# Kernel optimization log

Hardware: AMD Instinct MI355X
Metric: run time of the kernel (lower is better)

The kernel has to match this reference:

```python
import jax, jax.numpy as jnp
import numpy as np

D_FEAT = 6
HIDDEN = 64
NEG_SLOPE = 0.01  # torch LeakyReLU default


def gru_layer(x, Wih, Whh, bih, bhh):
    # x: [N, T, D] -> outputs [N, T, H], PyTorch GRU gate math (r,z,n order)
    N = x.shape[0]
    H = Whh.shape[1]
    def step(h, xt):
        gi = xt @ Wih.T + bih          # [N, 3H]
        gh = h @ Whh.T + bhh           # [N, 3H]
        i_r, i_z, i_n = jnp.split(gi, 3, axis=-1)
        h_r, h_z, h_n = jnp.split(gh, 3, axis=-1)
        r = jax.nn.sigmoid(i_r + h_r)
        z = jax.nn.sigmoid(i_z + h_z)
        n = jnp.tanh(i_n + r * h_n)
        h_new = (1.0 - z) * n + z * h
        return h_new, h_new
    h0 = jnp.zeros((N, H), x.dtype)
    _, hs = jax.lax.scan(step, h0, jnp.swapaxes(x, 0, 1))  # hs: [T, N, H]
    return jnp.swapaxes(hs, 0, 1)


def setup_inputs() -> dict:
    key = jax.random.key(0)
    ks = jax.random.split(key, 16)
    N, T, D, H, R = 2048, 60, D_FEAT, HIDDEN, 20
    x = jax.random.normal(ks[0], (N, D * T), dtype=jnp.float32)
    vals = jax.random.uniform(ks[1], (N, N, R), dtype=jnp.float32)
    keep = jax.random.uniform(ks[2], (N, N, R), dtype=jnp.float32) < 0.3
    relation_matrix = vals * keep.astype(jnp.float32)
    s = 1.0 / np.sqrt(H)
    def u(k, shape):
        return jax.random.uniform(k, shape, dtype=jnp.float32, minval=-s, maxval=s)
    inp = {
        "x": x,
        "relation_matrix": relation_matrix,
        "Wih0": u(ks[3], (3 * H, D)),
        "Whh0": u(ks[4], (3 * H, H)),
        "bih0": u(ks[5], (3 * H,)),
        "bhh0": u(ks[6], (3 * H,)),
        "Wih1": u(ks[7], (3 * H, H)),
        "Whh1": u(ks[8], (3 * H, H)),
        "bih1": u(ks[9], (3 * H,)),
        "bhh1": u(ks[10], (3 * H,)),
        "W": jax.random.normal(ks[11], (2 * H + R, 1), dtype=jnp.float32) * 0.1,
        "b": jnp.zeros((1,), dtype=jnp.float32),
        "fc_w": u(ks[12], (1, H)),
        "fc_b": jnp.zeros((1,), dtype=jnp.float32),
    }
    return inp


def reference(x, relation_matrix, Wih0, Whh0, bih0, bhh0, Wih1, Whh1, bih1, bhh1, W, b, fc_w, fc_b):
    N = x.shape[0]
    H = HIDDEN
    R = relation_matrix.shape[2]
    # [N, d_feat*T] -> [N, T, d_feat]
    xs = jnp.transpose(x.reshape(N, D_FEAT, -1), (0, 2, 1))
    h = gru_layer(xs, Wih0, Whh0, bih0, bhh0)
    h = gru_layer(h, Wih1, Whh1, bih1, bhh1)
    x_hidden = h[:, -1, :]  # [N, H]
    # decompose concat @ W:  W = [W1 (ei part); W2 (hidden part); W3 (relation part)]
    W1 = W[:H, 0]
    W2 = W[H:2 * H, 0]
    W3 = W[2 * H:, 0]
    ai = x_hidden @ W1          # [N] contribution of row i
    aj = x_hidden @ W2          # [N] contribution of col j
    ar = jnp.einsum('ijr,r->ij', relation_matrix, W3)  # [N, N]
    weight = ai[:, None] + aj[None, :] + ar + b[0]
    weight = jnp.where(weight >= 0, weight, NEG_SLOPE * weight)  # leaky_relu
    mask = (jnp.sum(relation_matrix, axis=2) != 0).astype(x_hidden.dtype)
    valid_weight = mask * weight
    valid_weight = jax.nn.softmax(valid_weight, axis=1)
    hidden = valid_weight @ x_hidden  # [N, H]
    pred_all = ((hidden + x_hidden) @ fc_w.T + fc_b).squeeze(-1)  # [N]
    return pred_all
```

## Files before the change

kernel.cpp:

```cpp
#include <hip/hip_runtime.h>
#include <cstddef>

typedef __attribute__((ext_vector_type(8))) short short8;
typedef __attribute__((ext_vector_type(4))) float f32x4;

#define MFMA16(a, b, c) __builtin_amdgcn_mfma_f32_16x16x32_bf16((a), (b), (c), 0, 0, 0)

__device__ __forceinline__ unsigned short f2bf(float f) {
    unsigned u = __float_as_uint(f);
    u = (u + 0x7fffu + ((u >> 16) & 1u)) >> 16;
    return (unsigned short)u;
}
__device__ __forceinline__ float bf2f(unsigned short s) {
    return __uint_as_float(((unsigned)s) << 16);
}
__device__ __forceinline__ float sigm(float v) { return 1.f / (1.f + __expf(-v)); }
__device__ __forceinline__ float tanh_(float v) {
    float a = fabsf(v);
    float e = __expf(-2.f * a);
    float t = (1.f - e) / (1.f + e);
    return v < 0.f ? -t : t;
}

typedef __attribute__((address_space(1))) const void gas_t;
typedef __attribute__((address_space(3))) void las_t;
__device__ __forceinline__ void gld_lds16(const void* g, void* l) {
    __builtin_amdgcn_global_load_lds((gas_t*)g, (las_t*)l, 16, 0, 0);
}

__launch_bounds__(768, 3)
__global__ void gru_kernel(const float* __restrict__ x,
                           const float* __restrict__ Wih0, const float* __restrict__ Whh0,
                           const float* __restrict__ bih0, const float* __restrict__ bhh0,
                           const float* __restrict__ Wih1, const float* __restrict__ Whh1,
                           const float* __restrict__ bih1, const float* __restrict__ bhh1,
                           float* __restrict__ xhid) {
    __shared__ __align__(16) unsigned short h0h[2][1024], h0l[2][1024];
    __shared__ __align__(16) unsigned short h1h[2][1024], h1l[2][1024];
    __shared__ __align__(16) float P1[2][16][195];
    __shared__ __align__(16) short8 axbuf[2400];

    const int tid  = threadIdx.x;
    const int grp  = tid >> 8;
    const int lane = tid & 63;
    const int gw   = (tid >> 6) & 3;
    const int c    = lane & 15;
    const int q    = lane >> 4;
    const int jj   = gw * 16 + c;

    for (int i = tid; i < 1024; i += 768) {
        h0h[0][i] = 0; h0l[0][i] = 0; h1h[0][i] = 0; h1l[0][i] = 0;
    }
    {
        const float* xb = x + (size_t)blockIdx.x * 8 * 360;
        for (int f = tid; f < 1920; f += 768) {
            const int t = f >> 5, s = (f >> 2) & 7, qq = f & 3;
            unsigned short Hh[6], Ll[6];
#pragma unroll
            for (int d = 0; d < 6; ++d) {
                const float v = xb[s * 360 + d * 60 + t];
                Hh[d] = f2bf(v); Ll[d] = f2bf(v - bf2f(Hh[d]));
            }
            short8 fr;
#pragma unroll
            for (int e = 0; e < 8; ++e) {
                const int k = qq * 8 + e;
                unsigned short u = 0;
                if (k < 6) u = Hh[k];
                else if (k < 12) u = Ll[k - 6];
                else if (k < 18) u = Hh[k - 12];
                fr[e] = (short)u;
            }
            axbuf[t * 40 + s * 5 + qq] = fr;
        }
    }

    const int ka    = q * 8;
    const int swzA0 = c * 64 + (ka ^ ((c & 7) << 3));
    const int swzA1 = c * 64 + ((32 + ka) ^ ((c & 7) << 3));

    __syncthreads();

    if (grp == 0) {
        short8 Bhh[3][2], Bhl[3][2], Bc[3];
#pragma unroll
        for (int g = 0; g < 3; ++g) {
            const int o = g * 64 + jj;
#pragma unroll
            for (int kt = 0; kt < 2; ++kt) {
                const int k0 = kt * 32 + q * 8;
#pragma unroll
                for (int e = 0; e < 8; ++e) {
                    const float v = Whh0[o * 64 + k0 + e];
                    const unsigned short hi = f2bf(v);
                    Bhh[g][kt][e] = (short)hi; Bhl[g][kt][e] = (short)f2bf(v - bf2f(hi));
                }
            }
#pragma unroll
            for (int e = 0; e < 8; ++e) {
                const int ks = q * 8 + e;
                unsigned short bv = 0;
                if (ks < 6)       bv = f2bf(Wih0[o * 6 + ks]);
                else if (ks < 12) bv = f2bf(Wih0[o * 6 + ks - 6]);
                else if (ks < 18) {
                    const float v = Wih0[o * 6 + ks - 12];
                    const unsigned short hi = f2bf(v);
                    bv = f2bf(v - bf2f(hi));
                }
                Bc[g][e] = (short)bv;
            }
        }
        const float br = bih0[jj] + bhh0[jj];
        const float bz = bih0[64 + jj] + bhh0[64 + jj];
        const float bi = bih0[128 + jj];
        const float bh = bhh0[128 + jj];
        float hreg[4] = {0.f, 0.f, 0.f, 0.f};

        for (int it = 0; it < 62; ++it) {
            if (it < 60) {
                const int par = it & 1;
                const short8 ah0 = *(const short8*)&h0h[par][swzA0];
                const short8 ah1 = *(const short8*)&h0h[par][swzA1];
                const short8 al0 = *(const short8*)&h0l[par][swzA0];
                const short8 al1 = *(const short8*)&h0l[par][swzA1];
                const short8 ax  = axbuf[it * 40 + (c & 7) * 5 + q];

                f32x4 accr = {br, br, br, br};
                f32x4 accz = {bz, bz, bz, bz};
                f32x4 acci = {bi, bi, bi, bi};
                f32x4 acch = {bh, bh, bh, bh};

                accr = MFMA16(ah0, Bhh[0][0], accr); accr = MFMA16(ah1, Bhh[0][1], accr);
                accr = MFMA16(al0, Bhh[0][0], accr); accr = MFMA16(al1, Bhh[0][1], accr);
                accr = MFMA16(ah0, Bhl[0][0], accr); accr = MFMA16(ah1, Bhl[0][1], accr);
                accr = MFMA16(ax, Bc[0], accr);

                accz = MFMA16(ah0, Bhh[1][0], accz); accz = MFMA16(ah1, Bhh[1][1], accz);
                accz = MFMA16(al0, Bhh[1][0], accz); accz = MFMA16(al1, Bhh[1][1], accz);
                accz = MFMA16(ah0, Bhl[1][0], accz); accz = MFMA16(ah1, Bhl[1][1], accz);
                accz = MFMA16(ax, Bc[1], accz);

                acci = MFMA16(ax, Bc[2], acci);

                acch = MFMA16(ah0, Bhh[2][0], acch); acch = MFMA16(ah1, Bhh[2][1], acch);
                acch = MFMA16(al0, Bhh[2][0], acch); acch = MFMA16(al1, Bhh[2][1], acch);
                acch = MFMA16(ah0, Bhl[2][0], acch); acch = MFMA16(ah1, Bhl[2][1], acch);

#pragma unroll
                for (int i2 = 0; i2 < 4; ++i2) {
                    const float rr = sigm(accr[i2]);
                    const float zz = sigm(accz[i2]);
                    const float nn = tanh_(acci[i2] + rr * acch[i2]);
                    const float hv = (1.f - zz) * nn + zz * hreg[i2];
                    hreg[i2] = hv;
                    const int r  = q * 4 + i2;
                    const int ix = r * 64 + (jj ^ ((r & 7) << 3));
                    const unsigned short hi = f2bf(hv);
                    h0h[par ^ 1][ix] = hi;
                    h0l[par ^ 1][ix] = f2bf(hv - bf2f(hi));
                }
            }
            __syncthreads();
        }
    } else if (grp == 1) {
        short8 Bih[3][2], Bil[3][2];
#pragma unroll
        for (int g = 0; g < 3; ++g) {
            const int o = g * 64 + jj;
#pragma unroll
            for (int kt = 0; kt < 2; ++kt) {
                const int k0 = kt * 32 + q * 8;
#pragma unroll
                for (int e = 0; e < 8; ++e) {
                    const float v = Wih1[o * 64 + k0 + e];
                    const unsigned short hi = f2bf(v);
                    Bih[g][kt][e] = (short)hi; Bil[g][kt][e] = (short)f2bf(v - bf2f(hi));
                }
            }
        }
        const float br = bih1[jj] + bhh1[jj];
        const float bz = bih1[64 + jj] + bhh1[64 + jj];
        const float bi = bih1[128 + jj];

        for (int it = 0; it < 62; ++it) {
            if (it >= 1 && it < 61) {
                const int par = it & 1;
                const short8 gh0 = *(const short8*)&h0h[par][swzA0];
                const short8 gh1 = *(const short8*)&h0h[par][swzA1];
                const short8 gl0 = *(const short8*)&h0l[par][swzA0];
                const short8 gl1 = *(const short8*)&h0l[par][swzA1];

                f32x4 ar = {br, br, br, br};
                f32x4 az = {bz, bz, bz, bz};
                f32x4 an = {bi, bi, bi, bi};

                ar = MFMA16(gh0, Bih[0][0], ar); ar = MFMA16(gh1, Bih[0][1], ar);
                ar = MFMA16(gl0, Bih[0][0], ar); ar = MFMA16(gl1, Bih[0][1], ar);
                ar = MFMA16(gh0, Bil[0][0], ar); ar = MFMA16(gh1, Bil[0][1], ar);

                az = MFMA16(gh0, Bih[1][0], az); az = MFMA16(gh1, Bih[1][1], az);
                az = MFMA16(gl0, Bih[1][0], az); az = MFMA16(gl1, Bih[1][1], az);
                az = MFMA16(gh0, Bil[1][0], az); az = MFMA16(gh1, Bil[1][1], az);

                an = MFMA16(gh0, Bih[2][0], an); an = MFMA16(gh1, Bih[2][1], an);
                an = MFMA16(gl0, Bih[2][0], an); an = MFMA16(gl1, Bih[2][1], an);
                an = MFMA16(gh0, Bil[2][0], an); an = MFMA16(gh1, Bil[2][1], an);

#pragma unroll
                for (int i2 = 0; i2 < 4; ++i2) {
                    const int r = q * 4 + i2;
                    P1[par][r][jj]       = ar[i2];
                    P1[par][r][64 + jj]  = az[i2];
                    P1[par][r][128 + jj] = an[i2];
                }
            }
            __syncthreads();
        }
    } else {
        short8 Bhh[3][2], Bhl[3][2];
#pragma unroll
        for (int g = 0; g < 3; ++g) {
            const int o = g * 64 + jj;
#pragma unroll
            for (int kt = 0; kt < 2; ++kt) {
                const int k0 = kt * 32 + q * 8;
#pragma unroll
                for (int e = 0; e < 8; ++e) {
                    const float v = Whh1[o * 64 + k0 + e];
                    const unsigned short hi = f2bf(v);
                    Bhh[g][kt][e] = (short)hi; Bhl[g][kt][e] = (short)f2bf(v - bf2f(hi));
                }
            }
        }
        const float bh = bhh1[128 + jj];
        float hreg[4] = {0.f, 0.f, 0.f, 0.f};

        for (int it = 0; it < 62; ++it) {
            if (it >= 2) {
                const int par = it & 1;
                const short8 hh0 = *(const short8*)&h1h[par][swzA0];
                const short8 hh1_ = *(const short8*)&h1h[par][swzA1];
                const short8 hl0 = *(const short8*)&h1l[par][swzA0];
                const short8 hl1_ = *(const short8*)&h1l[par][swzA1];

                float p1r[4], p1z[4], p1n[4];
#pragma unroll
                for (int i2 = 0; i2 < 4; ++i2) {
                    const int r = q * 4 + i2;
                    p1r[i2] = P1[par ^ 1][r][jj];
                    p1z[i2] = P1[par ^ 1][r][64 + jj];
                    p1n[i2] = P1[par ^ 1][r][128 + jj];
                }

                f32x4 ar  = {p1r[0], p1r[1], p1r[2], p1r[3]};
                f32x4 az  = {p1z[0], p1z[1], p1z[2], p1z[3]};
                f32x4 ahn = {bh, bh, bh, bh};

                ar = MFMA16(hh0, Bhh[0][0], ar); ar = MFMA16(hh1_, Bhh[0][1], ar);
                ar = MFMA16(hl0, Bhh[0][0], ar); ar = MFMA16(hl1_, Bhh[0][1], ar);
                ar = MFMA16(hh0, Bhl[0][0], ar); ar = MFMA16(hh1_, Bhl[0][1], ar);

                az = MFMA16(hh0, Bhh[1][0], az); az = MFMA16(hh1_, Bhh[1][1], az);
                az = MFMA16(hl0, Bhh[1][0], az); az = MFMA16(hl1_, Bhh[1][1], az);
                az = MFMA16(hh0, Bhl[1][0], az); az = MFMA16(hh1_, Bhl[1][1], az);

                ahn = MFMA16(hh0, Bhh[2][0], ahn); ahn = MFMA16(hh1_, Bhh[2][1], ahn);
                ahn = MFMA16(hl0, Bhh[2][0], ahn); ahn = MFMA16(hl1_, Bhh[2][1], ahn);
                ahn = MFMA16(hh0, Bhl[2][0], ahn); ahn = MFMA16(hh1_, Bhl[2][1], ahn);

#pragma unroll
                for (int i2 = 0; i2 < 4; ++i2) {
                    const float rr = sigm(ar[i2]);
                    const float zz = sigm(az[i2]);
                    const float nn = tanh_(p1n[i2] + rr * ahn[i2]);
                    const float hv = (1.f - zz) * nn + zz * hreg[i2];
                    hreg[i2] = hv;
                    const int r  = q * 4 + i2;
                    const int ix = r * 64 + (jj ^ ((r & 7) << 3));
                    const unsigned short hi = f2bf(hv);
                    h1h[par ^ 1][ix] = hi;
                    h1l[par ^ 1][ix] = f2bf(hv - bf2f(hi));
                    if (it == 61 && q < 2)
                        xhid[((size_t)blockIdx.x * 8 + r) * 64 + jj] = hv;
                }
            }
            __syncthreads();
        }
    }
}

__global__ void aij_kernel(const float* __restrict__ xh, const float* __restrict__ W,
                           float* __restrict__ ai, float* __restrict__ aj) {
    const int n = blockIdx.x * 256 + threadIdx.x;
    const float* row = xh + (size_t)n * 64;
    float a1 = 0.f, a2 = 0.f;
#pragma unroll
    for (int k = 0; k < 64; k += 4) {
        const f32x4 v = *(const f32x4*)(row + k);
#pragma unroll
        for (int u = 0; u < 4; ++u) {
            a1 += v[u] * W[k + u];
            a2 += v[u] * W[64 + k + u];
        }
    }
    ai[n] = a1;
    aj[n] = a2;
}

__launch_bounds__(256, 2)
__global__ void rel_kernel(const float* __restrict__ rel, const float* __restrict__ xh,
                           const float* __restrict__ ai, const float* __restrict__ aj,
                           const float* __restrict__ W, const float* __restrict__ bptr,
                           const float* __restrict__ fcw, const float* __restrict__ fcb,
                           float* __restrict__ out) {
    __shared__ __align__(16) unsigned char stage[2][2][10240];
    __shared__ __align__(16) float pexp[2][2048];
    __shared__ __align__(16) float aj_s[2048];
    __shared__ float w3b_s[24];
    __shared__ float hidpart[4][2][64];
    __shared__ float redm[2][2], reds[2][2], rinv_s[2];

    const int tid  = threadIdx.x;
    const int lane = tid & 63;
    const int wv   = tid >> 6;
    const int i0   = blockIdx.x * 2;

    for (int k = tid; k < 2048; k += 256) aj_s[k] = aj[k];
    if (tid < 20) w3b_s[tid] = W[128 + tid];
    if (tid == 20) w3b_s[20] = bptr[0];
    if (tid < 2)  w3b_s[21 + tid] = ai[i0 + tid];
    __syncthreads();

    float w3[20];
#pragma unroll
    for (int r = 0; r < 20; ++r) w3[r] = w3b_s[r];
    const float bb  = w3b_s[20];
    const float aiv = (tid >> 7) ? w3b_s[22] : w3b_s[21];

    const int r_ = tid >> 7;
    const int t7 = tid & 127;

#pragma unroll
    for (int k = 0; k < 5; ++k) {
        const int m = wv + 4 * k;
        const int rr = m / 10, oo = (m % 10) * 1024;
        const unsigned char* g =
            (const unsigned char*)(rel + (size_t)(i0 + rr) * 2048 * 20) + oo + lane * 16;
        gld_lds16(g, &stage[0][rr][oo]);
    }

    for (int c = 0; c < 16; ++c) {
        const int buf = c & 1;
        if (c < 15) {
#pragma unroll
            for (int k = 0; k < 5; ++k) {
                const int m = wv + 4 * k;
                const int rr = m / 10, oo = (m % 10) * 1024;
                const unsigned char* g =
                    (const unsigned char*)(rel + ((size_t)(i0 + rr) * 2048 + (size_t)(c + 1) * 128) * 20)
                    + oo + lane * 16;
                gld_lds16(g, &stage[buf ^ 1][rr][oo]);
            }
            asm volatile("s_waitcnt vmcnt(5)" ::: "memory");
        } else {
            asm volatile("s_waitcnt vmcnt(0)" ::: "memory");
        }
        __builtin_amdgcn_s_barrier();
        __builtin_amdgcn_sched_barrier(0);

        const unsigned char* sp = &stage[buf][r_][t7 * 80];
        float arv = 0.f, ms = 0.f;
#pragma unroll
        for (int e = 0; e < 5; ++e) {
            const f32x4 v = *(const f32x4*)(sp + e * 16);
            arv += v[0] * w3[e * 4] + v[1] * w3[e * 4 + 1]
                 + v[2] * w3[e * 4 + 2] + v[3] * w3[e * 4 + 3];
            ms += v[0] + v[1] + v[2] + v[3];
        }
        const int j = c * 128 + t7;
        float wvv = aiv + aj_s[j] + arv + bb;
        wvv = (wvv >= 0.f) ? wvv : 0.01f * wvv;
        pexp[r_][j] = (ms != 0.f) ? wvv : 0.f;
        __builtin_amdgcn_s_barrier();
    }
    __syncthreads();

    const int c7 = tid & 127;
    const int wh = (tid >> 6) & 1;
    float mx = -1e30f;
#pragma unroll
    for (int m = 0; m < 16; ++m) mx = fmaxf(mx, pexp[r_][c7 + 128 * m]);
#pragma unroll
    for (int d = 1; d < 64; d <<= 1) mx = fmaxf(mx, __shfl_xor(mx, d, 64));
    if (lane == 0) redm[r_][wh] = mx;
    __syncthreads();
    mx = fmaxf(redm[r_][0], redm[r_][1]);

    float sm = 0.f;
#pragma unroll
    for (int m = 0; m < 16; ++m) {
        const int k = c7 + 128 * m;
        const float e = __expf(pexp[r_][k] - mx);
        pexp[r_][k] = e;
        sm += e;
    }
#pragma unroll
    for (int d = 1; d < 64; d <<= 1) sm += __shfl_xor(sm, d, 64);
    if (lane == 0) reds[r_][wh] = sm;
    __syncthreads();
    if (tid < 2) rinv_s[tid] = 1.f / (reds[tid][0] + reds[tid][1]);
    __syncthreads();

    const int col = lane;
    const int k0s = wv * 512;
    float acc0 = 0.f, acc1 = 0.f;
    for (int k = 0; k < 512; k += 4) {
        const float v0 = xh[(size_t)(k0s + k) * 64 + col];
        const float v1 = xh[(size_t)(k0s + k + 1) * 64 + col];
        const float v2 = xh[(size_t)(k0s + k + 2) * 64 + col];
        const float v3 = xh[(size_t)(k0s + k + 3) * 64 + col];
        const f32x4 e0 = *(const f32x4*)&pexp[0][k0s + k];
        const f32x4 e1 = *(const f32x4*)&pexp[1][k0s + k];
        acc0 += e0[0] * v0 + e0[1] * v1 + e0[2] * v2 + e0[3] * v3;
        acc1 += e1[0] * v0 + e1[1] * v1 + e1[2] * v2 + e1[3] * v3;
    }
    hidpart[wv][0][col] = acc0;
    hidpart[wv][1][col] = acc1;
    __syncthreads();

    if (tid < 128) {
        const int r2 = tid >> 6, cl = lane;
        float hs = hidpart[0][r2][cl] + hidpart[1][r2][cl]
                 + hidpart[2][r2][cl] + hidpart[3][r2][cl];
        const float h = hs * rinv_s[r2] + xh[(size_t)(i0 + r2) * 64 + cl];
        float p = h * fcw[cl];
#pragma unroll
        for (int d = 1; d < 64; d <<= 1) p += __shfl_xor(p, d, 64);
        if (cl == 0) out[i0 + r2] = p + fcb[0];
    }
}

extern "C" void kernel_launch(void* const* d_in, const int* in_sizes, int n_in,
                              void* d_out, int out_size, void* d_ws, size_t ws_size,
                              hipStream_t stream) {
    const float* x    = (const float*)d_in[0];
    const float* rel  = (const float*)d_in[1];
    const float* Wih0 = (const float*)d_in[2];
    const float* Whh0 = (const float*)d_in[3];
    const float* bih0 = (const float*)d_in[4];
    const float* bhh0 = (const float*)d_in[5];
    const float* Wih1 = (const float*)d_in[6];
    const float* Whh1 = (const float*)d_in[7];
    const float* bih1 = (const float*)d_in[8];
    const float* bhh1 = (const float*)d_in[9];
    const float* W    = (const float*)d_in[10];
    const float* b    = (const float*)d_in[11];
    const float* fcw  = (const float*)d_in[12];
    const float* fcb  = (const float*)d_in[13];
    float* out = (float*)d_out;

    float* xh = (float*)d_ws;
    float* ai = xh + 2048 * 64;
    float* aj = ai + 2048;

    gru_kernel<<<256, 768, 0, stream>>>(x, Wih0, Whh0, bih0, bhh0,
                                        Wih1, Whh1, bih1, bhh1, xh);
    aij_kernel<<<8, 256, 0, stream>>>(xh, W, ai, aj);
    rel_kernel<<<1024, 256, 0, stream>>>(rel, xh, ai, aj, W, b, fcw, fcb, out);
}
```

Baseline: 187.7 us.

## Overlap relation-tensor streaming with GRU recurrence in a fused kernel

Adds a fourth 256-thread group to the GRU kernel that streams the 335MB relation tensor during the latency-bound recurrence. It computes the per-edge relation dot product and a nonzero bitmask, and writes both to workspace. The final kernel then reads only the compact ar values and bitmask to run the softmax and aggregation. The aim is to hide the memory-bound relation pass behind the serial GRU steps, at the cost of extra workspace traffic (16MB ar plus mask), a 1024-thread block with lower occupancy, and lockstep barriers that tie the streaming rate to the GRU iteration count.

```diff
diff --git a/kernel.cpp b/kernel.cpp
--- a/kernel.cpp
+++ b/kernel.cpp
@@ -22,23 +22,68 @@
     return v < 0.f ? -t : t;
 }
 
-typedef __attribute__((address_space(1))) const void gas_t;
-typedef __attribute__((address_space(3))) void las_t;
-__device__ __forceinline__ void gld_lds16(const void* g, void* l) {
-    __builtin_amdgcn_global_load_lds((gas_t*)g, (las_t*)l, 16, 0, 0);
-}
-
-__launch_bounds__(768, 3)
-__global__ void gru_kernel(const float* __restrict__ x,
-                           const float* __restrict__ Wih0, const float* __restrict__ Whh0,
-                           const float* __restrict__ bih0, const float* __restrict__ bhh0,
-                           const float* __restrict__ Wih1, const float* __restrict__ Whh1,
-                           const float* __restrict__ bih1, const float* __restrict__ bhh1,
-                           float* __restrict__ xhid) {
+__device__ __forceinline__ void bar_lgkm() {
+    __builtin_amdgcn_sched_barrier(0);
+    asm volatile("s_waitcnt lgkmcnt(0)" ::: "memory");
+    __builtin_amdgcn_s_barrier();
+    __builtin_amdgcn_sched_barrier(0);
+}
+
+__device__ __forceinline__ void rel_issue(const float* __restrict__ rel, int bid, int rw,
+                                          int lane, int m,
+                                          f32x4& R0, f32x4& R1, f32x4& R2, f32x4& R3, f32x4& R4) {
+    const int task = bid * 16 + rw * 4 + (m >> 4);
+    const int row  = task >> 1;
+    const int j0   = (task & 1) * 1024 + (m & 15) * 64;
+    const float* gp = rel + ((size_t)row * 2048 + j0) * 20 + lane * 4;
+    R0 = *(const f32x4*)(gp);
+    R1 = *(const f32x4*)(gp + 256);
+    R2 = *(const f32x4*)(gp + 512);
+    R3 = *(const f32x4*)(gp + 768);
+    R4 = *(const f32x4*)(gp + 1024);
+}
+
+__device__ __forceinline__ void rel_consume(float* __restrict__ arw,
+                                            unsigned long long* __restrict__ maskw,
+                                            float (&buf)[1280], const float (&w3r)[20],
+                                            int bid, int rw, int lane, int m,
+                                            const f32x4& R0, const f32x4& R1, const f32x4& R2,
+                                            const f32x4& R3, const f32x4& R4) {
+    *(f32x4*)&buf[0    + lane * 4] = R0;
+    *(f32x4*)&buf[256  + lane * 4] = R1;
+    *(f32x4*)&buf[512  + lane * 4] = R2;
+    *(f32x4*)&buf[768  + lane * 4] = R3;
+    *(f32x4*)&buf[1024 + lane * 4] = R4;
+    float arv = 0.f, ms = 0.f;
+#pragma unroll
+    for (int e = 0; e < 5; ++e) {
+        const f32x4 v = *(const f32x4*)&buf[lane * 20 + e * 4];
+        arv += v[0] * w3r[e * 4] + v[1] * w3r[e * 4 + 1]
+             + v[2] * w3r[e * 4 + 2] + v[3] * w3r[e * 4 + 3];
+        ms  += v[0] + v[1] + v[2] + v[3];
+    }
+    const int task = bid * 16 + rw * 4 + (m >> 4);
+    const int row  = task >> 1;
+    const int j0   = (task & 1) * 1024 + (m & 15) * 64;
+    arw[(size_t)row * 2048 + j0 + lane] = arv;
+    const unsigned long long bal = __ballot(ms != 0.f);
+    if (lane == 0) maskw[(size_t)row * 32 + (j0 >> 6)] = bal;
+}
+
+__launch_bounds__(1024)
+__global__ void fused_kernel(const float* __restrict__ x,
+                             const float* __restrict__ Wih0, const float* __restrict__ Whh0,
+                             const float* __restrict__ bih0, const float* __restrict__ bhh0,
+                             const float* __restrict__ Wih1, const float* __restrict__ Whh1,
+                             const float* __restrict__ bih1, const float* __restrict__ bhh1,
+                             const float* __restrict__ rel, const float* __restrict__ W,
+                             float* __restrict__ xhid, float* __restrict__ arw,
+                             unsigned long long* __restrict__ maskw) {
     __shared__ __align__(16) unsigned short h0h[2][1024], h0l[2][1024];
     __shared__ __align__(16) unsigned short h1h[2][1024], h1l[2][1024];
     __shared__ __align__(16) float P1[2][16][195];
     __shared__ __align__(16) short8 axbuf[2400];
+    __shared__ __align__(16) float relbuf[4][1280];
 
     const int tid  = threadIdx.x;
     const int grp  = tid >> 8;
@@ -48,12 +93,12 @@
     const int q    = lane >> 4;
     const int jj   = gw * 16 + c;
 
-    for (int i = tid; i < 1024; i += 768) {
+    for (int i = tid; i < 1024; i += 1024) {
         h0h[0][i] = 0; h0l[0][i] = 0; h1h[0][i] = 0; h1l[0][i] = 0;
     }
     {
         const float* xb = x + (size_t)blockIdx.x * 8 * 360;
-        for (int f = tid; f < 1920; f += 768) {
+        for (int f = tid; f < 1920; f += 1024) {
             const int t = f >> 5, s = (f >> 2) & 7, qq = f & 3;
             unsigned short Hh[6], Ll[6];
 #pragma unroll
@@ -78,8 +123,6 @@
     const int ka    = q * 8;
     const int swzA0 = c * 64 + (ka ^ ((c & 7) << 3));
     const int swzA1 = c * 64 + ((32 + ka) ^ ((c & 7) << 3));
-
-    __syncthreads();
 
     if (grp == 0) {
         short8 Bhh[3][2], Bhl[3][2], Bc[3];
@@ -116,7 +159,8 @@
         const float bh = bhh0[128 + jj];
         float hreg[4] = {0.f, 0.f, 0.f, 0.f};
 
-        for (int it = 0; it < 62; ++it) {
+        __syncthreads();
+        for (int it = 0; it < 64; ++it) {
             if (it < 60) {
                 const int par = it & 1;
                 const short8 ah0 = *(const short8*)&h0h[par][swzA0];
@@ -160,7 +204,7 @@
                     h0l[par ^ 1][ix] = f2bf(hv - bf2f(hi));
                 }
             }
-            __syncthreads();
+            bar_lgkm();
         }
     } else if (grp == 1) {
         short8 Bih[3][2], Bil[3][2];
@@ -182,7 +226,8 @@
         const float bz = bih1[64 + jj] + bhh1[64 + jj];
         const float bi = bih1[128 + jj];
 
-        for (int it = 0; it < 62; ++it) {
+        __syncthreads();
+        for (int it = 0; it < 64; ++it) {
             if (it >= 1 && it < 61) {
                 const int par = it & 1;
                 const short8 gh0 = *(const short8*)&h0h[par][swzA0];
@@ -214,9 +259,9 @@
                     P1[par][r][128 + jj] = an[i2];
                 }
             }
-            __syncthreads();
-        }
-    } else {
+            bar_lgkm();
+        }
+    } else if (grp == 2) {
         short8 Bhh[3][2], Bhl[3][2];
 #pragma unroll
         for (int g = 0; g < 3; ++g) {
@@ -235,8 +280,9 @@
         const float bh = bhh1[128 + jj];
         float hreg[4] = {0.f, 0.f, 0.f, 0.f};
 
-        for (int it = 0; it < 62; ++it) {
-            if (it >= 2) {
+        __syncthreads();
+        for (int it = 0; it < 64; ++it) {
+            if (it >= 2 && it < 62) {
                 const int par = it & 1;
                 const short8 hh0 = *(const short8*)&h1h[par][swzA0];
                 const short8 hh1_ = *(const short8*)&h1h[par][swzA1];
@@ -284,7 +330,31 @@
                         xhid[((size_t)blockIdx.x * 8 + r) * 64 + jj] = hv;
                 }
             }
-            __syncthreads();
+            bar_lgkm();
+        }
+    } else {
+        const int rw  = (tid >> 6) - 12;
+        const int bid = blockIdx.x;
+        float w3r[20];
+#pragma unroll
+        for (int e = 0; e < 20; ++e) w3r[e] = W[128 + e];
+
+        f32x4 A0, A1, A2, A3, A4, B0, B1, B2, B3, B4;
+        rel_issue(rel, bid, rw, lane, 0, A0, A1, A2, A3, A4);
+
+        __syncthreads();
+        for (int it = 0; it < 64; ++it) {
+            const int mn = (it < 63) ? it + 1 : 63;
+            if ((it & 1) == 0) {
+                rel_issue(rel, bid, rw, lane, mn, B0, B1, B2, B3, B4);
+                rel_consume(arw, maskw, relbuf[rw], w3r, bid, rw, lane, it,
+                            A0, A1, A2, A3, A4);
+            } else {
+                rel_issue(rel, bid, rw, lane, mn, A0, A1, A2, A3, A4);
+                rel_consume(arw, maskw, relbuf[rw], w3r, bid, rw, lane, it,
+                            B0, B1, B2, B3, B4);
+            }
+            bar_lgkm();
         }
     }
 }
@@ -308,15 +378,13 @@
 }
 
 __launch_bounds__(256, 2)
-__global__ void rel_kernel(const float* __restrict__ rel, const float* __restrict__ xh,
-                           const float* __restrict__ ai, const float* __restrict__ aj,
-                           const float* __restrict__ W, const float* __restrict__ bptr,
-                           const float* __restrict__ fcw, const float* __restrict__ fcb,
-                           float* __restrict__ out) {
-    __shared__ __align__(16) unsigned char stage[2][2][10240];
+__global__ void finish_kernel(const float* __restrict__ arw,
+                              const unsigned long long* __restrict__ maskw,
+                              const float* __restrict__ xh, const float* __restrict__ ai,
+                              const float* __restrict__ aj, const float* __restrict__ bptr,
+                              const float* __restrict__ fcw, const float* __restrict__ fcb,
+                              float* __restrict__ out) {
     __shared__ __align__(16) float pexp[2][2048];
-    __shared__ __align__(16) float aj_s[2048];
-    __shared__ float w3b_s[24];
     __shared__ float hidpart[4][2][64];
     __shared__ float redm[2][2], reds[2][2], rinv_s[2];
 
@@ -324,72 +392,27 @@
     const int lane = tid & 63;
     const int wv   = tid >> 6;
     const int i0   = blockIdx.x * 2;
-
-    for (int k = tid; k < 2048; k += 256) aj_s[k] = aj[k];
-    if (tid < 20) w3b_s[tid] = W[128 + tid];
-    if (tid == 20) w3b_s[20] = bptr[0];
-    if (tid < 2)  w3b_s[21 + tid] = ai[i0 + tid];
+    const int r_   = tid >> 7;
+    const int t7   = tid & 127;
+
+    const float bb   = bptr[0];
+    const float aivr = ai[i0 + r_];
+
+#pragma unroll
+    for (int jc = 0; jc < 16; ++jc) {
+        const int j = jc * 128 + t7;
+        const float s = arw[(size_t)(i0 + r_) * 2048 + j];
+        const unsigned long long mw = maskw[(size_t)(i0 + r_) * 32 + (j >> 6)];
+        float wvv = aivr + aj[j] + s + bb;
+        wvv = (wvv >= 0.f) ? wvv : 0.01f * wvv;
+        pexp[r_][j] = ((mw >> (j & 63)) & 1ull) ? wvv : 0.f;
+    }
     __syncthreads();
 
-    float w3[20];
-#pragma unroll
-    for (int r = 0; r < 20; ++r) w3[r] = w3b_s[r];
-    const float bb  = w3b_s[20];
-    const float aiv = (tid >> 7) ? w3b_s[22] : w3b_s[21];
-
-    const int r_ = tid >> 7;
-    const int t7 = tid & 127;
-
-#pragma unroll
-    for (int k = 0; k < 5; ++k) {
-        const int m = wv + 4 * k;
-        const int rr = m / 10, oo = (m % 10) * 1024;
-        const unsigned char* g =
-            (const unsigned char*)(rel + (size_t)(i0 + rr) * 2048 * 20) + oo + lane * 16;
-        gld_lds16(g, &stage[0][rr][oo]);
-    }
-
-    for (int c = 0; c < 16; ++c) {
-        const int buf = c & 1;
-        if (c < 15) {
-#pragma unroll
-            for (int k = 0; k < 5; ++k) {
-                const int m = wv + 4 * k;
-                const int rr = m / 10, oo = (m % 10) * 1024;
-                const unsigned char* g =
-                    (const unsigned char*)(rel + ((size_t)(i0 + rr) * 2048 + (size_t)(c + 1) * 128) * 20)
-                    + oo + lane * 16;
-                gld_lds16(g, &stage[buf ^ 1][rr][oo]);
-            }
-            asm volatile("s_waitcnt vmcnt(5)" ::: "memory");
-        } else {
-            asm volatile("s_waitcnt vmcnt(0)" ::: "memory");
-        }
-        __builtin_amdgcn_s_barrier();
-        __builtin_amdgcn_sched_barrier(0);
-
-        const unsigned char* sp = &stage[buf][r_][t7 * 80];
-        float arv = 0.f, ms = 0.f;
-#pragma unroll
-        for (int e = 0; e < 5; ++e) {
-            const f32x4 v = *(const f32x4*)(sp + e * 16);
-            arv += v[0] * w3[e * 4] + v[1] * w3[e * 4 + 1]
-                 + v[2] * w3[e * 4 + 2] + v[3] * w3[e * 4 + 3];
-            ms += v[0] + v[1] + v[2] + v[3];
-        }
-        const int j = c * 128 + t7;
-        float wvv = aiv + aj_s[j] + arv + bb;
-        wvv = (wvv >= 0.f) ? wvv : 0.01f * wvv;
-        pexp[r_][j] = (ms != 0.f) ? wvv : 0.f;
-        __builtin_amdgcn_s_barrier();
-    }
-    __syncthreads();
-
-    const int c7 = tid & 127;
     const int wh = (tid >> 6) & 1;
     float mx = -1e30f;
 #pragma unroll
-    for (int m = 0; m < 16; ++m) mx = fmaxf(mx, pexp[r_][c7 + 128 * m]);
+    for (int m = 0; m < 16; ++m) mx = fmaxf(mx, pexp[r_][t7 + 128 * m]);
 #pragma unroll
     for (int d = 1; d < 64; d <<= 1) mx = fmaxf(mx, __shfl_xor(mx, d, 64));
     if (lane == 0) redm[r_][wh] = mx;
@@ -399,7 +422,7 @@
     float sm = 0.f;
 #pragma unroll
     for (int m = 0; m < 16; ++m) {
-        const int k = c7 + 128 * m;
+        const int k = t7 + 128 * m;
         const float e = __expf(pexp[r_][k] - mx);
         pexp[r_][k] = e;
         sm += e;
@@ -460,11 +483,14 @@
     float* out = (float*)d_out;
 
     float* xh = (float*)d_ws;
-    float* ai = xh + 2048 * 64;
+    float* ai = xh + 131072;
     float* aj = ai + 2048;
-
-    gru_kernel<<<256, 768, 0, stream>>>(x, Wih0, Whh0, bih0, bhh0,
-                                        Wih1, Whh1, bih1, bhh1, xh);
+    float* arw = aj + 2048;
+    unsigned long long* maskw = (unsigned long long*)(arw + 4194304);
+
+    fused_kernel<<<256, 1024, 0, stream>>>(x, Wih0, Whh0, bih0, bhh0,
+                                           Wih1, Whh1, bih1, bhh1,
+                                           rel, W, xh, arw, maskw);
     aij_kernel<<<8, 256, 0, stream>>>(xh, W, ai, aj);
-    rel_kernel<<<1024, 256, 0, stream>>>(rel, xh, ai, aj, W, b, fcw, fcb, out);
-}
+    finish_kernel<<<1024, 256, 0, stream>>>(arw, maskw, xh, ai, aj, b, fcw, fcb, out);
+}
```

Result: no change. 190.4 us (+1.5%).
